# Kernel optimization log

Measured on AMD Instinct MI355X. Metric: run time of the kernel, lower is better.

Reference implementation:

```python
import jax, jax.numpy as jnp
import numpy as np

L, H, D, HS = 6, 8, 512, 64
EPS = 1e-5


def _ln(x, g, b):
    m = jnp.mean(x, -1, keepdims=True)
    v = jnp.mean((x - m) ** 2, -1, keepdims=True)
    return (x - m) * jax.lax.rsqrt(v + EPS) * g + b


def _posenc(T, C):
    pos = jnp.arange(T, dtype=jnp.float32)[:, None]
    div = jnp.exp(jnp.arange(0, C, 2, dtype=jnp.float32) * (-jnp.log(10000.0) / C))
    pe = jnp.zeros((T, C), jnp.float32)
    pe = pe.at[:, 0::2].set(jnp.sin(pos * div))
    pe = pe.at[:, 1::2].set(jnp.cos(pos * div))
    return pe


def setup_inputs() -> dict:
    B, T, F, V, E, O = 8, 1024, 32, 7, 16, 49
    key = jax.random.key(0)
    ks = jax.random.split(key, 16)
    s = 0.02
    inp = {
        'code': jax.random.randint(ks[0], (B, T, F), 0, V),
        'lengths': jax.random.randint(ks[1], (B,), T // 2, T + 1),
        'emb': s * jax.random.normal(ks[2], (V, E), jnp.float32),
        'Wq': s * jax.random.normal(ks[3], (L, H, D, HS), jnp.float32),
        'Wk': s * jax.random.normal(ks[4], (L, H, D, HS), jnp.float32),
        'Wv': s * jax.random.normal(ks[5], (L, H, D, HS), jnp.float32),
        'Wo': s * jax.random.normal(ks[6], (L, D, D), jnp.float32),
        'bo': jnp.zeros((L, D), jnp.float32),
        'W1': s * jax.random.normal(ks[7], (L, D, 4 * D), jnp.float32),
        'b1': jnp.zeros((L, 4 * D), jnp.float32),
        'W2': s * jax.random.normal(ks[8], (L, 4 * D, D), jnp.float32),
        'b2': jnp.zeros((L, D), jnp.float32),
        'ln1_g': jnp.ones((L, D), jnp.float32),
        'ln1_b': jnp.zeros((L, D), jnp.float32),
        'ln2_g': jnp.ones((L, D), jnp.float32),
        'ln2_b': jnp.zeros((L, D), jnp.float32),
        'lnf_g': jnp.ones((D,), jnp.float32),
        'lnf_b': jnp.zeros((D,), jnp.float32),
        'attn_w': s * jax.random.normal(ks[9], (D, 1), jnp.float32),
        'attn_b': jnp.zeros((1,), jnp.float32),
        'head_w': s * jax.random.normal(ks[10], (D, 49), jnp.float32),
        'head_b': jnp.zeros((49,), jnp.float32),
    }
    return inp


def reference(code, lengths, emb, Wq, Wk, Wv, Wo, bo, W1, b1, W2, b2,
              ln1_g, ln1_b, ln2_g, ln2_b, lnf_g, lnf_b,
              attn_w, attn_b, head_w, head_b):
    B, T, F = code.shape
    # token embedding (B,T,F,E) -> (B,T,D) plus sinusoidal positions
    x = emb[code].reshape(B, T, D) + _posenc(T, D)
    mask = jnp.arange(T) < lengths[:, None]          # (B,T) valid positions
    col_mask = mask[:, None, None, :]                # mask key columns
    row_mask = mask[:, None, :, None]                # zero padded query rows
    for l in range(L):
        xn = _ln(x, ln1_g[l], ln1_b[l])
        q = jnp.einsum('btd,hde->bhte', xn, Wq[l])
        k = jnp.einsum('btd,hde->bhte', xn, Wk[l])
        v = jnp.einsum('btd,hde->bhte', xn, Wv[l])
        wei = jnp.einsum('bhte,bhse->bhts', q, k) * (HS ** -0.5)
        wei = jnp.where(col_mask, wei, -jnp.inf)
        wei = jax.nn.softmax(wei, axis=-1)
        wei = jnp.where(row_mask, wei, 0.0)
        o = jnp.einsum('bhts,bhse->bthe', wei, v).reshape(B, T, H * HS)
        x = x + o @ Wo[l] + bo[l]
        xn = _ln(x, ln2_g[l], ln2_b[l])
        x = x + jax.nn.gelu(xn @ W1[l] + b1[l], approximate=False) @ W2[l] + b2[l]
    x = _ln(x, lnf_g, lnf_b)
    # attention pooling over time
    scores = x @ attn_w + attn_b                     # (B,T,1)
    scores = jnp.where(mask[:, :, None], scores, -jnp.inf)
    aw = jax.nn.softmax(scores, axis=1)
    summary = jnp.sum(aw * x, axis=1)                # (B,D)
    logits = summary @ head_w + head_b               # (B,49)
    return logits
```

## Files before the change

kernel.cpp:

```cpp
#include <hip/hip_runtime.h>
#include <math.h>

#define TT 1024
#define BB 8
#define DD 512
#define HH 8
#define HSZ 64
#define LL 6
#define FF4 2048

typedef __attribute__((ext_vector_type(8))) short short8;
typedef __attribute__((ext_vector_type(4))) float floatx4;
typedef unsigned short ushort_t;
typedef unsigned int uint_t;

__device__ __forceinline__ ushort_t f2bf(float f) {
  uint_t u = __float_as_uint(f);
  u += 0x7fff + ((u >> 16) & 1);
  return (ushort_t)(u >> 16);
}
__device__ __forceinline__ float bf2f(ushort_t h) {
  return __uint_as_float(((uint_t)h) << 16);
}

#if defined(__has_builtin)
#if __has_builtin(__builtin_amdgcn_sched_group_barrier)
#define SGB(mask, n) __builtin_amdgcn_sched_group_barrier(mask, n, 0)
#endif
#endif
#ifndef SGB
#define SGB(mask, n)
#endif


__global__ __launch_bounds__(256) void k_embed(const int* __restrict__ code,
                                               const float* __restrict__ emb,
                                               float* __restrict__ x) {
  int idx = blockIdx.x * 256 + threadIdx.x;
  int c = idx & (DD - 1);
  int bt = idx >> 9;
  int t = bt & (TT - 1);
  int f = c >> 4, e = c & 15;
  int vv = code[bt * 32 + f];
  int i = c >> 1;
  float freq = expf((float)(2 * i) * (-9.210340371976184f / 512.f));
  float ang = (float)t * freq;
  float pe = (c & 1) ? cosf(ang) : sinf(ang);
  x[idx] = emb[vv * 16 + e] + pe;
}

__global__ __launch_bounds__(256) void k_ln(const float* __restrict__ x,
                                            ushort_t* __restrict__ yB,
                                            float* __restrict__ yF,
                                            const float* __restrict__ g,
                                            const float* __restrict__ b,
                                            const float* __restrict__ aw,
                                            const float* __restrict__ ab,
                                            float* __restrict__ scores) {
  int wave = threadIdx.x >> 6, lane = threadIdx.x & 63;
  int row = blockIdx.x * 4 + wave;
  const float* xr = x + (size_t)row * DD;
  float v[8];
  *(float4*)&v[0] = *(const float4*)(xr + lane * 8);
  *(float4*)&v[4] = *(const float4*)(xr + lane * 8 + 4);
  float s = 0.f;
#pragma unroll
  for (int j = 0; j < 8; ++j) s += v[j];
#pragma unroll
  for (int off = 32; off; off >>= 1) s += __shfl_down(s, off, 64);
  float mean = __shfl(s, 0, 64) * (1.f / DD);
  float qv = 0.f;
#pragma unroll
  for (int j = 0; j < 8; ++j) { float d = v[j] - mean; qv += d * d; }
#pragma unroll
  for (int off = 32; off; off >>= 1) qv += __shfl_down(qv, off, 64);
  float rs = rsqrtf(__shfl(qv, 0, 64) * (1.f / DD) + 1e-5f);
  float ov[8];
  float sdot = 0.f;
#pragma unroll
  for (int e = 0; e < 8; ++e) {
    int c = lane * 8 + e;
    ov[e] = (v[e] - mean) * rs * g[c] + b[c];
    if (scores) sdot += ov[e] * aw[c];
  }
  if (yB) {
    short8 o8;
#pragma unroll
    for (int e = 0; e < 8; ++e) o8[e] = (short)f2bf(ov[e]);
    size_t ad = (((size_t)(row >> 4) * 16 + (lane >> 2)) << 9) + ((lane & 3) * 16 + (row & 15)) * 8;
    *(short8*)(yB + ad) = o8;
  } else {
    float* yr = yF + (size_t)row * DD + lane * 8;
    *(float4*)yr = *(float4*)&ov[0];
    *(float4*)(yr + 4) = *(float4*)&ov[4];
  }
  if (scores) {
#pragma unroll
    for (int off = 32; off; off >>= 1) sdot += __shfl_down(sdot, off, 64);
    if (lane == 0) scores[row] = sdot + ab[0];
  }
}

__global__ __launch_bounds__(256) void k_packw(const float* __restrict__ in,
                                               ushort_t* __restrict__ out,
                                               int Nin, long in_ms, int nh,
                                               long os_l, int nblk, int Kout) {
  __shared__ float t4[64][65];
  int mz = blockIdx.z;
  const float* ip = in + (size_t)mz * in_ms;
  ushort_t* op = out + (size_t)(mz / nh) * os_l;
  int nbase = (mz % nh) * nblk + blockIdx.y * 64;
  int k0 = blockIdx.x * 64;
  int cc = threadIdx.x & 63, r0 = threadIdx.x >> 6;
#pragma unroll
  for (int i = 0; i < 16; ++i) {
    int r = r0 * 16 + i;
    t4[r][cc] = ip[(size_t)(k0 + r) * Nin + (nbase - (mz % nh) * nblk) + cc];
  }
  __syncthreads();
#pragma unroll
  for (int half = 0; half < 2; ++half) {
    int c = threadIdx.x + half * 256;
    int joct = c >> 6, nl = c & 63;
    int n = nbase + nl, k = k0 + joct * 8;
    short8 v8;
#pragma unroll
    for (int e = 0; e < 8; ++e) v8[e] = (short)f2bf(t4[joct * 8 + e][nl]);
    size_t ad = (((size_t)(n >> 4) * (Kout >> 5) + (k >> 5)) << 9) + (((k >> 3) & 3) * 16 + (n & 15)) * 8;
    *(short8*)(op + ad) = v8;
  }
}

template <int MT, int D>
__global__ __launch_bounds__(64, (MT == 4) ? 3 : 2) void k_pgemm(const ushort_t* __restrict__ Apk,
                                                                 const ushort_t* __restrict__ Bpk,
                                                                 const float* __restrict__ resid,
                                                                 const float* __restrict__ bias,
                                                                 float* __restrict__ outF,
                                                                 ushort_t* __restrict__ outB,
                                                                 int M, int N, int K, int mode,
                                                                 const int* __restrict__ lengths) {
  __shared__ ushort_t Cb[MT == 4 ? 64 * 80 : 64];
  const int lane = threadIdx.x;
  const int quad = lane >> 4, l16 = lane & 15;
  const int gx = N >> 6;
  int id = blockIdx.x;
  int bx = (id >> 3) % gx;
  int by = (id / (8 * gx)) * 8 + (id & 7);
  const int row0 = by * (MT * 16), col0 = bx * 64;
  if (lengths && (row0 & (TT - 1)) >= lengths[row0 >> 10]) return;
  const int nk = K >> 5;
  const ushort_t* Ab = Apk + (((size_t)(row0 >> 4) * nk) << 9) + lane * 8;
  const ushort_t* Bb = Bpk + (((size_t)(col0 >> 4) * nk) << 9) + lane * 8;
  floatx4 acc[MT][4] = {};
  short8 af[D][MT], bf[D][4];
#pragma unroll
  for (int d = 0; d < D; ++d) {
#pragma unroll
    for (int mt = 0; mt < MT; ++mt) af[d][mt] = *(const short8*)(Ab + (((size_t)(mt * nk + d)) << 9));
#pragma unroll
    for (int nt = 0; nt < 4; ++nt) bf[d][nt] = *(const short8*)(Bb + (((size_t)(nt * nk + d)) << 9));
  }
  int kc = 0;
  for (; kc + D < nk; kc += D) {
#pragma unroll
    for (int d = 0; d < D; ++d) {
#pragma unroll
      for (int mt = 0; mt < MT; ++mt)
#pragma unroll
        for (int nt = 0; nt < 4; ++nt)
          acc[mt][nt] = __builtin_amdgcn_mfma_f32_16x16x32_bf16(af[d][mt], bf[d][nt], acc[mt][nt], 0, 0, 0);
      SGB(0x008, MT * 4);
      const int nxt = kc + d + D;
#pragma unroll
      for (int mt = 0; mt < MT; ++mt) af[d][mt] = *(const short8*)(Ab + (((size_t)(mt * nk + nxt)) << 9));
#pragma unroll
      for (int nt = 0; nt < 4; ++nt) bf[d][nt] = *(const short8*)(Bb + (((size_t)(nt * nk + nxt)) << 9));
      SGB(0x020, MT + 4);
    }
  }
#pragma unroll
  for (int d = 0; d < D; ++d)
#pragma unroll
    for (int mt = 0; mt < MT; ++mt)
#pragma unroll
      for (int nt = 0; nt < 4; ++nt)
        acc[mt][nt] = __builtin_amdgcn_mfma_f32_16x16x32_bf16(af[d][mt], bf[d][nt], acc[mt][nt], 0, 0, 0);

  if (MT == 4 && mode == 2) {
#pragma unroll
    for (int mt = 0; mt < MT; ++mt)
#pragma unroll
      for (int nt = 0; nt < 4; ++nt) {
        floatx4 a4 = acc[mt][nt];
#pragma unroll
        for (int r = 0; r < 4; ++r) {
          float val = a4[r] + bias[col0 + nt * 16 + l16];
          val = 0.5f * val * (1.f + erff(val * 0.7071067811865475f));
          Cb[(mt * 16 + quad * 4 + r) * 80 + nt * 16 + l16] = f2bf(val);
        }
      }
#pragma unroll
    for (int mt2 = 0; mt2 < 4; ++mt2)
#pragma unroll
      for (int kt2 = 0; kt2 < 2; ++kt2) {
        short8 v8 = *(const short8*)&Cb[(mt2 * 16 + l16) * 80 + kt2 * 32 + quad * 8];
        size_t ad = ((((size_t)(row0 >> 4) + mt2) * (N >> 5) + (col0 >> 5) + kt2) << 9) + lane * 8;
        *(short8*)(outB + ad) = v8;
      }
  } else {
    const float qscale = (mode == 3 && col0 < 512) ? 0.125f : 1.0f;
#pragma unroll
    for (int mt = 0; mt < MT; ++mt)
#pragma unroll
      for (int nt = 0; nt < 4; ++nt) {
        floatx4 a4 = acc[mt][nt];
#pragma unroll
        for (int r = 0; r < 4; ++r) {
          int row = row0 + mt * 16 + quad * 4 + r;
          int col = col0 + nt * 16 + l16;
          float val = a4[r];
          if (bias) val += bias[col];
          size_t idx = (size_t)row * N + col;
          if (mode == 1) outF[idx] = val + resid[idx];
          else outB[idx] = f2bf(val * qscale);
        }
      }
  }
}

__global__ __launch_bounds__(256) void k_attn(const ushort_t* __restrict__ qkv,
                                              const int* __restrict__ lengths,
                                              ushort_t* __restrict__ o) {
  __shared__ ushort_t Ks[64 * 72];
  __shared__ ushort_t Vt[64 * 72];
  __shared__ ushort_t Ps[4][16 * 72];
  const int tid = threadIdx.x;
  const int w = tid >> 6, lane = tid & 63;
  const int quad = lane >> 4, l16 = lane & 15;
  const int tile = blockIdx.x & 15;
  const int bh = blockIdx.x >> 4;
  const int b = bh >> 3, h = bh & 7;
  const int len = lengths[b];
  if (tile * 64 >= len) return;
  const int tqa = tile * 64 + w * 16 + l16;
  const ushort_t* qp = qkv + ((size_t)(b * TT + tqa)) * 1536 + h * HSZ + quad * 8;
  short8 qf0 = *(const short8*)qp;
  short8 qf1 = *(const short8*)(qp + 32);
  floatx4 oacc[4] = {};
  float lsum[4] = {0.f, 0.f, 0.f, 0.f};
  const int skey = tid >> 2, sseg = (tid & 3) << 4;
  const int vkp = (tid & 31) << 1, vds = (tid >> 5) << 3;
  const int nkt = (len + 63) >> 6;
  for (int kt = 0; kt < nkt; ++kt) {
    const int s0 = kt * 64;
    __syncthreads();
    {
      const ushort_t* kp = qkv + ((size_t)(b * TT + s0 + skey)) * 1536 + 512 + h * HSZ + sseg;
      short8 k0 = *(const short8*)kp;
      short8 k1 = *(const short8*)(kp + 8);
      *(short8*)&Ks[skey * 72 + sseg] = k0;
      *(short8*)&Ks[skey * 72 + sseg + 8] = k1;
      const ushort_t* vp0 = qkv + ((size_t)(b * TT + s0 + vkp)) * 1536 + 1024 + h * HSZ + vds;
      short8 v0 = *(const short8*)vp0;
      short8 v1 = *(const short8*)(vp0 + 1536);
#pragma unroll
      for (int i = 0; i < 8; ++i) {
        ushort2 pr;
        pr.x = (ushort_t)v0[i];
        pr.y = (ushort_t)v1[i];
        *(ushort2*)&Vt[(vds + i) * 72 + vkp] = pr;
      }
    }
    __syncthreads();
    floatx4 sacc[4] = {};
#pragma unroll
    for (int nt = 0; nt < 4; ++nt) {
      short8 kf0 = *(const short8*)&Ks[(nt * 16 + l16) * 72 + quad * 8];
      short8 kf1 = *(const short8*)&Ks[(nt * 16 + l16) * 72 + 32 + quad * 8];
      sacc[nt] = __builtin_amdgcn_mfma_f32_16x16x32_bf16(qf0, kf0, sacc[nt], 0, 0, 0);
      sacc[nt] = __builtin_amdgcn_mfma_f32_16x16x32_bf16(qf1, kf1, sacc[nt], 0, 0, 0);
    }
    float p[4][4];
    if (kt == nkt - 1) {
#pragma unroll
      for (int nt = 0; nt < 4; ++nt) {
        bool valid = (s0 + nt * 16 + l16 < len);
#pragma unroll
        for (int r = 0; r < 4; ++r) p[nt][r] = valid ? __expf(sacc[nt][r]) : 0.f;
      }
    } else {
#pragma unroll
      for (int nt = 0; nt < 4; ++nt)
#pragma unroll
        for (int r = 0; r < 4; ++r) p[nt][r] = __expf(sacc[nt][r]);
    }
#pragma unroll
    for (int r = 0; r < 4; ++r)
#pragma unroll
      for (int nt = 0; nt < 4; ++nt) {
        lsum[r] += p[nt][r];
        Ps[w][(quad * 4 + r) * 72 + nt * 16 + l16] = f2bf(p[nt][r]);
      }
    short8 pf0 = *(const short8*)&Ps[w][l16 * 72 + quad * 8];
    short8 pf1 = *(const short8*)&Ps[w][l16 * 72 + 32 + quad * 8];
#pragma unroll
    for (int nt = 0; nt < 4; ++nt) {
      short8 vf0 = *(const short8*)&Vt[(nt * 16 + l16) * 72 + quad * 8];
      short8 vf1 = *(const short8*)&Vt[(nt * 16 + l16) * 72 + 32 + quad * 8];
      oacc[nt] = __builtin_amdgcn_mfma_f32_16x16x32_bf16(pf0, vf0, oacc[nt], 0, 0, 0);
      oacc[nt] = __builtin_amdgcn_mfma_f32_16x16x32_bf16(pf1, vf1, oacc[nt], 0, 0, 0);
    }
  }
#pragma unroll
  for (int off = 1; off < 16; off <<= 1) {
#pragma unroll
    for (int r = 0; r < 4; ++r) lsum[r] += __shfl_xor(lsum[r], off, 64);
  }
#pragma unroll
  for (int r = 0; r < 4; ++r) {
    int t = tile * 64 + w * 16 + quad * 4 + r;
    float inv = (t < len) ? 1.f / lsum[r] : 0.f;
#pragma unroll
    for (int nt = 0; nt < 4; ++nt)
      Ps[w][(quad * 4 + r) * 72 + nt * 16 + l16] = f2bf(oacc[nt][r] * inv);
  }
  const int mtile = b * 64 + tile * 4 + w;
#pragma unroll
  for (int kt2 = 0; kt2 < 2; ++kt2) {
    short8 v8 = *(const short8*)&Ps[w][l16 * 72 + kt2 * 32 + quad * 8];
    size_t ad = (((size_t)mtile * 16 + h * 2 + kt2) << 9) + lane * 8;
    *(short8*)(o + ad) = v8;
  }
}

__global__ __launch_bounds__(256) void k_softw(const float* __restrict__ scores,
                                               const int* __restrict__ lengths,
                                               float* __restrict__ wts) {
  __shared__ float red[8];
  int tid = threadIdx.x, b = blockIdx.x;
  int len = lengths[b];
  const float* sb = scores + b * TT;
  float m = -1e30f;
  for (int t = tid; t < len; t += 256) m = fmaxf(m, sb[t]);
#pragma unroll
  for (int off = 32; off; off >>= 1) m = fmaxf(m, __shfl_down(m, off, 64));
  if ((tid & 63) == 0) red[tid >> 6] = m;
  __syncthreads();
  m = fmaxf(fmaxf(red[0], red[1]), fmaxf(red[2], red[3]));
  float ssum = 0.f;
  for (int t = tid; t < len; t += 256) ssum += __expf(sb[t] - m);
#pragma unroll
  for (int off = 32; off; off >>= 1) ssum += __shfl_down(ssum, off, 64);
  if ((tid & 63) == 0) red[4 + (tid >> 6)] = ssum;
  __syncthreads();
  float inv = 1.f / (red[4] + red[5] + red[6] + red[7]);
  for (int t = tid; t < TT; t += 256)
    wts[b * TT + t] = (t < len) ? __expf(sb[t] - m) * inv : 0.f;
}

__global__ __launch_bounds__(256) void k_wsum(const float* __restrict__ xf,
                                              const float* __restrict__ wts,
                                              float* __restrict__ partial) {
  int b = blockIdx.x, c = blockIdx.y, tid = threadIdx.x;
  const float* xb = xf + ((size_t)b * TT + c * 64) * DD;
  const float* wb = wts + b * TT + c * 64;
  float a0 = 0.f, a1 = 0.f;
  for (int t = 0; t < 64; ++t) {
    float wv = wb[t];
    a0 += wv * xb[(size_t)t * DD + tid];
    a1 += wv * xb[(size_t)t * DD + tid + 256];
  }
  float* pp = partial + ((size_t)b * 16 + c) * DD;
  pp[tid] = a0;
  pp[tid + 256] = a1;
}

__global__ __launch_bounds__(64) void k_head(const float* __restrict__ partial,
                                             const float* __restrict__ head_w,
                                             const float* __restrict__ head_b,
                                             float* __restrict__ out) {
  __shared__ float ssum[DD];
  int b = blockIdx.x, tid = threadIdx.x;
  for (int d = tid; d < DD; d += 64) {
    float s = 0.f;
#pragma unroll
    for (int c = 0; c < 16; ++c) s += partial[((size_t)b * 16 + c) * DD + d];
    ssum[d] = s;
  }
  __syncthreads();
  if (tid < 49) {
    float s = head_b[tid];
    for (int d = 0; d < DD; ++d) s += ssum[d] * head_w[d * 49 + tid];
    out[b * 49 + tid] = s;
  }
}

extern "C" void kernel_launch(void* const* d_in, const int* in_sizes, int n_in,
                              void* d_out, int out_size, void* d_ws, size_t ws_size,
                              hipStream_t stream) {
  const int* code = (const int*)d_in[0];
  const int* lengths = (const int*)d_in[1];
  const float* emb = (const float*)d_in[2];
  const float* Wq = (const float*)d_in[3];
  const float* Wk = (const float*)d_in[4];
  const float* Wv = (const float*)d_in[5];
  const float* Wo = (const float*)d_in[6];
  const float* bo = (const float*)d_in[7];
  const float* W1 = (const float*)d_in[8];
  const float* b1 = (const float*)d_in[9];
  const float* W2 = (const float*)d_in[10];
  const float* b2 = (const float*)d_in[11];
  const float* ln1_g = (const float*)d_in[12];
  const float* ln1_b = (const float*)d_in[13];
  const float* ln2_g = (const float*)d_in[14];
  const float* ln2_b = (const float*)d_in[15];
  const float* lnf_g = (const float*)d_in[16];
  const float* lnf_b = (const float*)d_in[17];
  const float* attn_w = (const float*)d_in[18];
  const float* attn_b = (const float*)d_in[19];
  const float* head_w = (const float*)d_in[20];
  const float* head_b = (const float*)d_in[21];
  float* out = (float*)d_out;

  const size_t NTOK = (size_t)BB * TT;
  float* x = (float*)d_ws;
  ushort_t* xn = (ushort_t*)(x + NTOK * DD);
  ushort_t* un = xn + NTOK * DD;
  ushort_t* qkv = un;
  ushort_t* h1 = un;
  float* xf = (float*)un;
  ushort_t* wqpk = un + (size_t)NTOK * FF4;
  ushort_t* wopk = wqpk + (size_t)LL * 1536 * 512;
  ushort_t* w1pk = wopk + (size_t)LL * 512 * 512;
  ushort_t* w2pk = w1pk + (size_t)LL * 512 * FF4;
  float* scores = (float*)(w2pk + (size_t)LL * FF4 * 512);
  float* wts = scores + NTOK;
  float* partial = wts + NTOK;

  k_packw<<<dim3(8, 1, 48), 256, 0, stream>>>(Wq, wqpk,              64, (long)512 * 64, 8, (long)1536 * 512, 64, 512);
  k_packw<<<dim3(8, 1, 48), 256, 0, stream>>>(Wk, wqpk + 512 * 512,  64, (long)512 * 64, 8, (long)1536 * 512, 64, 512);
  k_packw<<<dim3(8, 1, 48), 256, 0, stream>>>(Wv, wqpk + 1024 * 512, 64, (long)512 * 64, 8, (long)1536 * 512, 64, 512);
  k_packw<<<dim3(8, 8, 6), 256, 0, stream>>>(Wo, wopk, 512, (long)512 * 512, 1, (long)512 * 512, 0, 512);
  k_packw<<<dim3(8, 32, 6), 256, 0, stream>>>(W1, w1pk, 2048, (long)512 * 2048, 1, (long)2048 * 512, 0, 512);
  k_packw<<<dim3(32, 8, 6), 256, 0, stream>>>(W2, w2pk, 512, (long)2048 * 512, 1, (long)512 * 2048, 0, 2048);

  k_embed<<<dim3((unsigned)((NTOK * DD) / 256)), dim3(256), 0, stream>>>(code, emb, x);

  for (int l = 0; l < LL; ++l) {
    k_ln<<<dim3(NTOK / 4), 256, 0, stream>>>(x, xn, nullptr, ln1_g + l * DD, ln1_b + l * DD,
                                             nullptr, nullptr, nullptr);
    k_pgemm<4, 2><<<dim3(24 * 128), 64, 0, stream>>>(xn, wqpk + (size_t)l * 1536 * 512, nullptr, nullptr,
                                                     nullptr, qkv, (int)NTOK, 1536, 512, 3, lengths);
    k_attn<<<dim3(BB * HH * (TT / 64)), 256, 0, stream>>>(qkv, lengths, xn);
    k_pgemm<2, 8><<<dim3(8 * 256), 64, 0, stream>>>(xn, wopk + (size_t)l * 512 * 512, x, bo + l * DD,
                                                    x, nullptr, (int)NTOK, 512, 512, 1, lengths);
    k_ln<<<dim3(NTOK / 4), 256, 0, stream>>>(x, xn, nullptr, ln2_g + l * DD, ln2_b + l * DD,
                                             nullptr, nullptr, nullptr);
    k_pgemm<4, 2><<<dim3(32 * 128), 64, 0, stream>>>(xn, w1pk + (size_t)l * 512 * FF4, nullptr, b1 + l * FF4,
                                                     nullptr, h1, (int)NTOK, FF4, 512, 2, lengths);
    k_pgemm<2, 8><<<dim3(8 * 256), 64, 0, stream>>>(h1, w2pk + (size_t)l * FF4 * 512, x, b2 + l * DD,
                                                    x, nullptr, (int)NTOK, 512, 2048, 1, lengths);
  }
  k_ln<<<dim3(NTOK / 4), 256, 0, stream>>>(x, nullptr, xf, lnf_g, lnf_b,
                                           attn_w, attn_b, scores);
  k_softw<<<dim3(BB), 256, 0, stream>>>(scores, lengths, wts);
  k_wsum<<<dim3(BB, 16), 256, 0, stream>>>(xf, wts, partial);
  k_head<<<dim3(BB), 64, 0, stream>>>(partial, head_w, head_b, out);
}
```

Measured before the change: 1.378 ms.

## Skip padded rows in embed/LN/wsum and retile Wo/W2 GEMMs to 32x32

Embedding, layernorm and the pooling partial-sum kernels now exit early for token rows beyond each sequence's length, so they stop doing work on padding. The GEMM kernel gains an NT template parameter. The Wo and W2 projections now use 32x32 tiles with a shallower prefetch depth, doubling the grid and raising the occupancy hint, which should spread the N=512 GEMMs across more CUs. Skipping padded rows leaves x, xn and xf uninitialized there. This relies on downstream consumers never reading those rows.

```diff
diff --git a/kernel.cpp b/kernel.cpp
--- a/kernel.cpp
+++ b/kernel.cpp
@@ -35,11 +35,13 @@
 
 __global__ __launch_bounds__(256) void k_embed(const int* __restrict__ code,
                                                const float* __restrict__ emb,
-                                               float* __restrict__ x) {
+                                               float* __restrict__ x,
+                                               const int* __restrict__ lengths) {
   int idx = blockIdx.x * 256 + threadIdx.x;
   int c = idx & (DD - 1);
   int bt = idx >> 9;
   int t = bt & (TT - 1);
+  if (t >= lengths[bt >> 10]) return;
   int f = c >> 4, e = c & 15;
   int vv = code[bt * 32 + f];
   int i = c >> 1;
@@ -56,9 +58,12 @@
                                             const float* __restrict__ b,
                                             const float* __restrict__ aw,
                                             const float* __restrict__ ab,
-                                            float* __restrict__ scores) {
+                                            float* __restrict__ scores,
+                                            const int* __restrict__ lengths) {
+  int row0 = blockIdx.x * 4;
+  if ((row0 & (TT - 1)) >= lengths[row0 >> 10]) return;
   int wave = threadIdx.x >> 6, lane = threadIdx.x & 63;
-  int row = blockIdx.x * 4 + wave;
+  int row = row0 + wave;
   const float* xr = x + (size_t)row * DD;
   float v[8];
   *(float4*)&v[0] = *(const float4*)(xr + lane * 8);
@@ -131,8 +136,8 @@
   }
 }
 
-template <int MT, int D>
-__global__ __launch_bounds__(64, (MT == 4) ? 3 : 2) void k_pgemm(const ushort_t* __restrict__ Apk,
+template <int MT, int NT, int D>
+__global__ __launch_bounds__(64, (MT == 4) ? 3 : 4) void k_pgemm(const ushort_t* __restrict__ Apk,
                                                                  const ushort_t* __restrict__ Bpk,
                                                                  const float* __restrict__ resid,
                                                                  const float* __restrict__ bias,
@@ -143,23 +148,23 @@
   __shared__ ushort_t Cb[MT == 4 ? 64 * 80 : 64];
   const int lane = threadIdx.x;
   const int quad = lane >> 4, l16 = lane & 15;
-  const int gx = N >> 6;
+  const int gx = N / (NT * 16);
   int id = blockIdx.x;
   int bx = (id >> 3) % gx;
   int by = (id / (8 * gx)) * 8 + (id & 7);
-  const int row0 = by * (MT * 16), col0 = bx * 64;
+  const int row0 = by * (MT * 16), col0 = bx * (NT * 16);
   if (lengths && (row0 & (TT - 1)) >= lengths[row0 >> 10]) return;
   const int nk = K >> 5;
   const ushort_t* Ab = Apk + (((size_t)(row0 >> 4) * nk) << 9) + lane * 8;
   const ushort_t* Bb = Bpk + (((size_t)(col0 >> 4) * nk) << 9) + lane * 8;
-  floatx4 acc[MT][4] = {};
-  short8 af[D][MT], bf[D][4];
+  floatx4 acc[MT][NT] = {};
+  short8 af[D][MT], bf[D][NT];
 #pragma unroll
   for (int d = 0; d < D; ++d) {
 #pragma unroll
     for (int mt = 0; mt < MT; ++mt) af[d][mt] = *(const short8*)(Ab + (((size_t)(mt * nk + d)) << 9));
 #pragma unroll
-    for (int nt = 0; nt < 4; ++nt) bf[d][nt] = *(const short8*)(Bb + (((size_t)(nt * nk + d)) << 9));
+    for (int nt = 0; nt < NT; ++nt) bf[d][nt] = *(const short8*)(Bb + (((size_t)(nt * nk + d)) << 9));
   }
   int kc = 0;
   for (; kc + D < nk; kc += D) {
@@ -168,15 +173,15 @@
 #pragma unroll
       for (int mt = 0; mt < MT; ++mt)
 #pragma unroll
-        for (int nt = 0; nt < 4; ++nt)
+        for (int nt = 0; nt < NT; ++nt)
           acc[mt][nt] = __builtin_amdgcn_mfma_f32_16x16x32_bf16(af[d][mt], bf[d][nt], acc[mt][nt], 0, 0, 0);
-      SGB(0x008, MT * 4);
+      SGB(0x008, MT * NT);
       const int nxt = kc + d + D;
 #pragma unroll
       for (int mt = 0; mt < MT; ++mt) af[d][mt] = *(const short8*)(Ab + (((size_t)(mt * nk + nxt)) << 9));
 #pragma unroll
-      for (int nt = 0; nt < 4; ++nt) bf[d][nt] = *(const short8*)(Bb + (((size_t)(nt * nk + nxt)) << 9));
-      SGB(0x020, MT + 4);
+      for (int nt = 0; nt < NT; ++nt) bf[d][nt] = *(const short8*)(Bb + (((size_t)(nt * nk + nxt)) << 9));
+      SGB(0x020, MT + NT);
     }
   }
 #pragma unroll
@@ -184,14 +189,14 @@
 #pragma unroll
     for (int mt = 0; mt < MT; ++mt)
 #pragma unroll
-      for (int nt = 0; nt < 4; ++nt)
+      for (int nt = 0; nt < NT; ++nt)
         acc[mt][nt] = __builtin_amdgcn_mfma_f32_16x16x32_bf16(af[d][mt], bf[d][nt], acc[mt][nt], 0, 0, 0);
 
   if (MT == 4 && mode == 2) {
 #pragma unroll
     for (int mt = 0; mt < MT; ++mt)
 #pragma unroll
-      for (int nt = 0; nt < 4; ++nt) {
+      for (int nt = 0; nt < NT; ++nt) {
         floatx4 a4 = acc[mt][nt];
 #pragma unroll
         for (int r = 0; r < 4; ++r) {
@@ -213,7 +218,7 @@
 #pragma unroll
     for (int mt = 0; mt < MT; ++mt)
 #pragma unroll
-      for (int nt = 0; nt < 4; ++nt) {
+      for (int nt = 0; nt < NT; ++nt) {
         floatx4 a4 = acc[mt][nt];
 #pragma unroll
         for (int r = 0; r < 4; ++r) {
@@ -361,8 +366,15 @@
 
 __global__ __launch_bounds__(256) void k_wsum(const float* __restrict__ xf,
                                               const float* __restrict__ wts,
-                                              float* __restrict__ partial) {
+                                              float* __restrict__ partial,
+                                              const int* __restrict__ lengths) {
   int b = blockIdx.x, c = blockIdx.y, tid = threadIdx.x;
+  float* pp = partial + ((size_t)b * 16 + c) * DD;
+  if (c * 64 >= lengths[b]) {
+    pp[tid] = 0.f;
+    pp[tid + 256] = 0.f;
+    return;
+  }
   const float* xb = xf + ((size_t)b * TT + c * 64) * DD;
   const float* wb = wts + b * TT + c * 64;
   float a0 = 0.f, a1 = 0.f;
@@ -371,7 +383,6 @@
     a0 += wv * xb[(size_t)t * DD + tid];
     a1 += wv * xb[(size_t)t * DD + tid + 256];
   }
-  float* pp = partial + ((size_t)b * 16 + c) * DD;
   pp[tid] = a0;
   pp[tid + 256] = a1;
 }
@@ -445,26 +456,26 @@
   k_packw<<<dim3(8, 32, 6), 256, 0, stream>>>(W1, w1pk, 2048, (long)512 * 2048, 1, (long)2048 * 512, 0, 512);
   k_packw<<<dim3(32, 8, 6), 256, 0, stream>>>(W2, w2pk, 512, (long)2048 * 512, 1, (long)512 * 2048, 0, 2048);
 
-  k_embed<<<dim3((unsigned)((NTOK * DD) / 256)), dim3(256), 0, stream>>>(code, emb, x);
+  k_embed<<<dim3((unsigned)((NTOK * DD) / 256)), dim3(256), 0, stream>>>(code, emb, x, lengths);
 
   for (int l = 0; l < LL; ++l) {
     k_ln<<<dim3(NTOK / 4), 256, 0, stream>>>(x, xn, nullptr, ln1_g + l * DD, ln1_b + l * DD,
-                                             nullptr, nullptr, nullptr);
-    k_pgemm<4, 2><<<dim3(24 * 128), 64, 0, stream>>>(xn, wqpk + (size_t)l * 1536 * 512, nullptr, nullptr,
-                                                     nullptr, qkv, (int)NTOK, 1536, 512, 3, lengths);
+                                             nullptr, nullptr, nullptr, lengths);
+    k_pgemm<4, 4, 2><<<dim3(24 * 128), 64, 0, stream>>>(xn, wqpk + (size_t)l * 1536 * 512, nullptr, nullptr,
+                                                        nullptr, qkv, (int)NTOK, 1536, 512, 3, lengths);
     k_attn<<<dim3(BB * HH * (TT / 64)), 256, 0, stream>>>(qkv, lengths, xn);
-    k_pgemm<2, 8><<<dim3(8 * 256), 64, 0, stream>>>(xn, wopk + (size_t)l * 512 * 512, x, bo + l * DD,
-                                                    x, nullptr, (int)NTOK, 512, 512, 1, lengths);
+    k_pgemm<2, 2, 4><<<dim3(16 * 256), 64, 0, stream>>>(xn, wopk + (size_t)l * 512 * 512, x, bo + l * DD,
+                                                        x, nullptr, (int)NTOK, 512, 512, 1, lengths);
     k_ln<<<dim3(NTOK / 4), 256, 0, stream>>>(x, xn, nullptr, ln2_g + l * DD, ln2_b + l * DD,
-                                             nullptr, nullptr, nullptr);
-    k_pgemm<4, 2><<<dim3(32 * 128), 64, 0, stream>>>(xn, w1pk + (size_t)l * 512 * FF4, nullptr, b1 + l * FF4,
-                                                     nullptr, h1, (int)NTOK, FF4, 512, 2, lengths);
-    k_pgemm<2, 8><<<dim3(8 * 256), 64, 0, stream>>>(h1, w2pk + (size_t)l * FF4 * 512, x, b2 + l * DD,
-                                                    x, nullptr, (int)NTOK, 512, 2048, 1, lengths);
+                                             nullptr, nullptr, nullptr, lengths);
+    k_pgemm<4, 4, 2><<<dim3(32 * 128), 64, 0, stream>>>(xn, w1pk + (size_t)l * 512 * FF4, nullptr, b1 + l * FF4,
+                                                        nullptr, h1, (int)NTOK, FF4, 512, 2, lengths);
+    k_pgemm<2, 2, 4><<<dim3(16 * 256), 64, 0, stream>>>(h1, w2pk + (size_t)l * FF4 * 512, x, b2 + l * DD,
+                                                        x, nullptr, (int)NTOK, 512, 2048, 1, lengths);
   }
   k_ln<<<dim3(NTOK / 4), 256, 0, stream>>>(x, nullptr, xf, lnf_g, lnf_b,
-                                           attn_w, attn_b, scores);
+                                           attn_w, attn_b, scores, lengths);
   k_softw<<<dim3(BB), 256, 0, stream>>>(scores, lengths, wts);
-  k_wsum<<<dim3(BB, 16), 256, 0, stream>>>(xf, wts, partial);
+  k_wsum<<<dim3(BB, 16), 256, 0, stream>>>(xf, wts, partial, lengths);
   k_head<<<dim3(BB), 64, 0, stream>>>(partial, head_w, head_b, out);
 }
```

After: 1.350 ms. -2.0%, faster.
